# Performance work log

Hardware: AMD Instinct MI355X
Metric: run time of the kernel (lower is better)

## Reference

```python
import jax, jax.numpy as jnp
import numpy as np

N = 262144      # total atoms (ragged over batch)
B = 64          # batch_size
K = 16          # retrieved features per sample
H = 256         # h_dim
R = 512         # ret_feat_dim


def setup_inputs() -> dict:
    key = jax.random.key(0)
    k1, k2, k3, k4, k5, k6, k7 = jax.random.split(key, 7)
    h = jax.random.normal(k1, (N, H), dtype=jnp.float32)
    ret_feat = jax.random.normal(k2, (B, K, R), dtype=jnp.float32)
    batch = jnp.sort(jax.random.randint(k3, (N,), 0, B, dtype=jnp.int64))
    # nn.Linear weights: y = x @ W.T + b
    Wp = jax.random.normal(k4, (H, R), dtype=jnp.float32) / np.sqrt(R)
    bp = jax.random.normal(k5, (H,), dtype=jnp.float32) * 0.01
    Wl = jax.random.normal(k6, (H, 2 * H), dtype=jnp.float32) / np.sqrt(2 * H)
    bl = jax.random.normal(k7, (H,), dtype=jnp.float32) * 0.01
    return {"h": h, "ret_feat": ret_feat, "batch": batch,
            "Wp": Wp, "bp": bp, "Wl": Wl, "bl": bl}


def reference(h, ret_feat, batch, Wp, bp, Wl, bl):
    # ret_feat: [B, K, R] -> mean over K -> project to [B, H]
    ret = jnp.mean(ret_feat, axis=1)                    # [B, R]
    ret = ret @ Wp.T + bp                               # [B, H]
    # The torch loop gathers h[batch==i], concats the pooled feature
    # repeated per atom, applies `linear`, and scatters back. Since every
    # atom is covered exactly once, this is a per-node gather + linear:
    per_node = ret[batch]                               # [N, H] gather
    x = jnp.concatenate([h, per_node], axis=-1)         # [N, 2H]
    return x @ Wl.T + bl                                # [N, H]
```

## Files before the change

### kernel.cpp

```cpp
#include <hip/hip_runtime.h>
#include <hip/hip_bf16.h>

#define N_ATOMS 262144
#define B_SZ    64
#define H_DIM   256
#define R_DIM   512

#define TILE_ROWS 16
#define TPB       32
#define NBLOCKS   (N_ATOMS / (TILE_ROWS * TPB))
#define NBUF      4

typedef __attribute__((ext_vector_type(8))) short bf16x8;
typedef __attribute__((ext_vector_type(4))) float f32x4;

static __device__ __forceinline__ short f2bf(float f) {
  unsigned u = __builtin_bit_cast(unsigned, f);
  u = (u + 0x7FFFu + ((u >> 16) & 1u)) >> 16;
  return (short)u;
}

static __device__ __forceinline__ unsigned cvtpk(float lo, float hi) {
  unsigned r;
  asm("v_cvt_pk_bf16_f32 %0, %1, %2" : "=v"(r) : "v"(lo), "v"(hi));
  return r;
}

static __device__ __forceinline__ bf16x8 pack8(f32x4 a0, f32x4 a1) {
  unsigned u0 = cvtpk(a0[0], a0[1]);
  unsigned u1 = cvtpk(a0[2], a0[3]);
  unsigned u2 = cvtpk(a1[0], a1[1]);
  unsigned u3 = cvtpk(a1[2], a1[3]);
  bf16x8 v;
  v[0] = (short)(u0 & 0xFFFF); v[1] = (short)(u0 >> 16);
  v[2] = (short)(u1 & 0xFFFF); v[3] = (short)(u1 >> 16);
  v[4] = (short)(u2 & 0xFFFF); v[5] = (short)(u2 >> 16);
  v[6] = (short)(u3 & 0xFFFF); v[7] = (short)(u3 >> 16);
  return v;
}

static __device__ __forceinline__ void async_copy16(const float* g, short* lds) {
  __builtin_amdgcn_global_load_lds(
      (const __attribute__((address_space(1))) unsigned int*)g,
      (__attribute__((address_space(3))) unsigned int*)lds,
      16, 0, 0);
}

__global__ __launch_bounds__(1024) void prep_kernel(
    const float* __restrict__ rf, const float* __restrict__ Wp,
    const float* __restrict__ bp, const float* __restrict__ Wl,
    const float* __restrict__ bl, float* __restrict__ pooled,
    short* __restrict__ Bbf) {
  int t = threadIdx.x;
  if (blockIdx.x >= B_SZ) {
    int base = (blockIdx.x - B_SZ) * 4096 + t * 4;
#pragma unroll
    for (int q = 0; q < 4; ++q) {
      int idx  = base + q;
      int j    = idx & 7;
      int lane = (idx >> 3) & 63;
      int ks   = (idx >> 9) & 7;
      int ct   = idx >> 12;
      int o    = ct * 16 + (lane & 15);
      int k    = ks * 32 + ((lane >> 4) << 3) + j;
      Bbf[idx] = f2bf(Wl[o * (2 * H_DIM) + k]);
    }
    return;
  }

  __shared__ float meanr[R_DIM];
  __shared__ float retj[H_DIM];
  int b    = blockIdx.x;
  int lane = t & 63;
  int w    = t >> 6;

  if (t < R_DIM) {
    float s = 0.f;
    const float* p = rf + (long)b * 16 * R_DIM + t;
#pragma unroll
    for (int k = 0; k < 16; ++k) s += p[k * R_DIM];
    meanr[t] = s * (1.f / 16.f);
  }
  __syncthreads();

  {
    f32x4 m0 = *(const f32x4*)&meanr[lane * 8];
    f32x4 m1 = *(const f32x4*)&meanr[lane * 8 + 4];
#pragma unroll
    for (int jj = 0; jj < 16; ++jj) {
      int j = w * 16 + jj;
      const f32x4* wp = (const f32x4*)(Wp + (long)j * R_DIM + lane * 8);
      f32x4 w0 = wp[0], w1 = wp[1];
      float s = m0[0]*w0[0] + m0[1]*w0[1] + m0[2]*w0[2] + m0[3]*w0[3]
              + m1[0]*w1[0] + m1[1]*w1[1] + m1[2]*w1[2] + m1[3]*w1[3];
#pragma unroll
      for (int d = 1; d < 64; d <<= 1) s += __shfl_xor(s, d);
      if (lane == 0) retj[j] = s + bp[j];
    }
  }
  __syncthreads();

  {
    f32x4 r0 = *(const f32x4*)&retj[lane * 4];
#pragma unroll
    for (int oo = 0; oo < 16; ++oo) {
      int o = w * 16 + oo;
      f32x4 wv = *(const f32x4*)(Wl + (long)o * (2 * H_DIM) + H_DIM + lane * 4);
      float s = r0[0]*wv[0] + r0[1]*wv[1] + r0[2]*wv[2] + r0[3]*wv[3];
#pragma unroll
      for (int d = 1; d < 64; d <<= 1) s += __shfl_xor(s, d);
      if (lane == 0) pooled[b * H_DIM + o] = s + bl[o];
    }
  }
}

__global__ __launch_bounds__(512, 4) void gemm_kernel(
    const float* __restrict__ h, const short* __restrict__ Bbf,
    const float* __restrict__ pooled, const int* __restrict__ batch,
    float* __restrict__ out) {
  __shared__ short As[NBUF][16 * 512];
  __shared__ float pooled_lds[8 * 256];
  __shared__ short boff_lds[512];
  __shared__ short scratch[512];
  int t    = threadIdx.x;
  int lane = t & 63;
  int w    = t >> 6;
  const int arow = lane & 15;
  const int kg   = lane >> 4;

  bf16x8 bfrag0[8], bfrag1[8];
#pragma unroll
  for (int ks = 0; ks < 8; ++ks) {
    bfrag0[ks] = *(const bf16x8*)(Bbf + ((((2 * w)     * 8 + ks) * 64 + lane) << 3));
    bfrag1[ks] = *(const bf16x8*)(Bbf + ((((2 * w + 1) * 8 + ks) * 64 + lane) << 3));
  }

  long base_row = (long)blockIdx.x * (TILE_ROWS * TPB);
  int o0 = (w << 5) + (kg << 2);
  int o1 = o0 + 16;
  const long lsrc = (long)arow * H_DIM + (w << 5) + (kg << 3);

  int b_t     = batch[base_row + t];
  int b_first = batch[base_row];
  int b_last  = batch[base_row + 511];
  int span    = b_last - b_first + 1;

#pragma unroll
  for (int tl = 0; tl < 3; ++tl) {
    const float* gp = h + (base_row + (long)tl * TILE_ROWS) * H_DIM + lsrc;
    async_copy16(gp,     &As[tl][(2 * w) * 512]);
    async_copy16(gp + 4, &As[tl][(2 * w + 1) * 512]);
  }

  boff_lds[t] = (short)(b_t - b_first);
  if (span <= 8) {
    int fi = t * 4;
    if (fi < span * H_DIM)
      *(f32x4*)&pooled_lds[fi] =
          *(const f32x4*)(pooled + (long)b_first * H_DIM + fi);
  }
  asm volatile("s_waitcnt vmcnt(0) lgkmcnt(0)" ::: "memory");
  __builtin_amdgcn_s_barrier();
  __builtin_amdgcn_sched_barrier(0);

  const bool small_span = (span <= 8);

  for (int tt = 0; tt < TPB; ++tt) {
    long g0 = base_row + (long)tt * TILE_ROWS;

    {
      const float* gp;
      short *d0, *d1;
      if (tt + 3 < TPB) {
        gp = h + (g0 + 3 * TILE_ROWS) * H_DIM + lsrc;
        short* dbuf = &As[(tt + 3) & 3][0];
        d0 = dbuf + (2 * w) * 512;
        d1 = dbuf + (2 * w + 1) * 512;
      } else {
        gp = h + base_row * H_DIM + lsrc;
        d0 = scratch;
        d1 = scratch;
      }
      async_copy16(gp,     d0);
      async_copy16(gp + 4, d1);
    }
    __builtin_amdgcn_sched_barrier(0);
    asm volatile("s_waitcnt vmcnt(10)" ::: "memory");
    __builtin_amdgcn_sched_barrier(0);

    const short* ab = &As[tt & 3][0];
    f32x4 acc0 = {0.f, 0.f, 0.f, 0.f};
    f32x4 acc1 = {0.f, 0.f, 0.f, 0.f};
#pragma unroll
    for (int ks = 0; ks < 8; ++ks) {
      f32x4 v0 = *(const f32x4*)(ab + ks * 1024 + lane * 8);
      f32x4 v1 = *(const f32x4*)(ab + ks * 1024 + 512 + lane * 8);
      bf16x8 af = pack8(v0, v1);
      acc0 = __builtin_amdgcn_mfma_f32_16x16x32_bf16(bfrag0[ks], af, acc0, 0, 0, 0);
      acc1 = __builtin_amdgcn_mfma_f32_16x16x32_bf16(bfrag1[ks], af, acc1, 0, 0, 0);
    }

    int off = (int)boff_lds[tt * 16 + arow];
    f32x4 pv0, pv1;
    if (small_span) {
      pv0 = *(const f32x4*)&pooled_lds[(off << 8) + o0];
      pv1 = *(const f32x4*)&pooled_lds[(off << 8) + o1];
    } else {
      const float* pb = pooled + (long)(b_first + off) * H_DIM;
      pv0 = *(const f32x4*)(pb + o0);
      pv1 = *(const f32x4*)(pb + o1);
    }

    float* orow = out + (g0 + arow) * H_DIM;
    *(f32x4*)(orow + o0) = acc0 + pv0;
    *(f32x4*)(orow + o1) = acc1 + pv1;

    __builtin_amdgcn_s_barrier();
    __builtin_amdgcn_sched_barrier(0);
  }
}

extern "C" void kernel_launch(void* const* d_in, const int* in_sizes, int n_in,
                              void* d_out, int out_size, void* d_ws, size_t ws_size,
                              hipStream_t stream) {
  const float* h   = (const float*)d_in[0];
  const float* rf  = (const float*)d_in[1];
  const int*   bat = (const int*)d_in[2];
  const float* Wp  = (const float*)d_in[3];
  const float* bp  = (const float*)d_in[4];
  const float* Wl  = (const float*)d_in[5];
  const float* bl  = (const float*)d_in[6];
  float* out = (float*)d_out;

  float* pooled = (float*)d_ws;
  short* Bbf    = (short*)((char*)d_ws + 64 * 1024);

  prep_kernel<<<B_SZ + 16, 1024, 0, stream>>>(rf, Wp, bp, Wl, bl, pooled, Bbf);
  gemm_kernel<<<NBLOCKS, 512, 0, stream>>>(h, Bbf, pooled, bat, out);
}
```

Before: 144.8 us.

## Halve GEMM block to 4 waves, each computing four 16-column output tiles

The GEMM block shrinks from 512 to 256 threads. Each wave now holds B fragments for four 16-wide column tiles instead of two, so every converted bf16 A fragment feeds four MFMAs rather than two, and each wave loads twice as much of each h tile. The vmcnt wait moves from before the MFMA loop to after the stores, just before the barrier, so global loads can overlap more work. In exchange, register pressure rises to 128 VGPRs of B fragments, and the same LDS footprint per block means fewer resident waves per CU for hiding latency.

```diff
diff --git a/kernel.cpp b/kernel.cpp
--- a/kernel.cpp
+++ b/kernel.cpp
@@ -114,7 +114,7 @@
   }
 }
 
-__global__ __launch_bounds__(512, 4) void gemm_kernel(
+__global__ __launch_bounds__(256, 2) void gemm_kernel(
     const float* __restrict__ h, const short* __restrict__ Bbf,
     const float* __restrict__ pooled, const int* __restrict__ batch,
     float* __restrict__ out) {
@@ -128,93 +128,96 @@
   const int arow = lane & 15;
   const int kg   = lane >> 4;
 
-  bf16x8 bfrag0[8], bfrag1[8];
-#pragma unroll
-  for (int ks = 0; ks < 8; ++ks) {
-    bfrag0[ks] = *(const bf16x8*)(Bbf + ((((2 * w)     * 8 + ks) * 64 + lane) << 3));
-    bfrag1[ks] = *(const bf16x8*)(Bbf + ((((2 * w + 1) * 8 + ks) * 64 + lane) << 3));
-  }
+  bf16x8 bfrag[4][8];
+#pragma unroll
+  for (int ci = 0; ci < 4; ++ci)
+#pragma unroll
+    for (int ks = 0; ks < 8; ++ks)
+      bfrag[ci][ks] = *(const bf16x8*)(
+          Bbf + ((((4 * w + ci) * 8 + ks) * 64 + lane) << 3));
 
   long base_row = (long)blockIdx.x * (TILE_ROWS * TPB);
-  int o0 = (w << 5) + (kg << 2);
-  int o1 = o0 + 16;
-  const long lsrc = (long)arow * H_DIM + (w << 5) + (kg << 3);
+  const long lsrc = (long)arow * H_DIM + (w << 6) + (kg << 3);
 
   int b_t     = batch[base_row + t];
+  int b_t2    = batch[base_row + 256 + t];
   int b_first = batch[base_row];
-  int b_last  = batch[base_row + 511];
+  int b_last  = batch[base_row + TILE_ROWS * TPB - 1];
   int span    = b_last - b_first + 1;
-
+  boff_lds[t]       = (short)(b_t  - b_first);
+  boff_lds[t + 256] = (short)(b_t2 - b_first);
+  const bool small_span = (span <= 8);
+  if (small_span) {
+    int fi = t * 8;
+    if (fi < span * H_DIM) {
+      *(f32x4*)&pooled_lds[fi]     = *(const f32x4*)(pooled + (long)b_first * H_DIM + fi);
+      *(f32x4*)&pooled_lds[fi + 4] = *(const f32x4*)(pooled + (long)b_first * H_DIM + fi + 4);
+    }
+  }
 #pragma unroll
   for (int tl = 0; tl < 3; ++tl) {
     const float* gp = h + (base_row + (long)tl * TILE_ROWS) * H_DIM + lsrc;
-    async_copy16(gp,     &As[tl][(2 * w) * 512]);
-    async_copy16(gp + 4, &As[tl][(2 * w + 1) * 512]);
-  }
-
-  boff_lds[t] = (short)(b_t - b_first);
-  if (span <= 8) {
-    int fi = t * 4;
-    if (fi < span * H_DIM)
-      *(f32x4*)&pooled_lds[fi] =
-          *(const f32x4*)(pooled + (long)b_first * H_DIM + fi);
-  }
-  asm volatile("s_waitcnt vmcnt(0) lgkmcnt(0)" ::: "memory");
-  __builtin_amdgcn_s_barrier();
-  __builtin_amdgcn_sched_barrier(0);
-
-  const bool small_span = (span <= 8);
+    short* d = &As[tl][0];
+    async_copy16(gp,      d + (4 * w)     * 512);
+    async_copy16(gp + 4,  d + (4 * w + 1) * 512);
+    async_copy16(gp + 32, d + (4 * w + 2) * 512);
+    async_copy16(gp + 36, d + (4 * w + 3) * 512);
+  }
+  __syncthreads();
 
   for (int tt = 0; tt < TPB; ++tt) {
     long g0 = base_row + (long)tt * TILE_ROWS;
 
     {
       const float* gp;
-      short *d0, *d1;
+      short *d0, *d1, *d2, *d3;
       if (tt + 3 < TPB) {
         gp = h + (g0 + 3 * TILE_ROWS) * H_DIM + lsrc;
-        short* dbuf = &As[(tt + 3) & 3][0];
-        d0 = dbuf + (2 * w) * 512;
-        d1 = dbuf + (2 * w + 1) * 512;
+        short* d = &As[(tt + 3) & 3][0];
+        d0 = d + (4 * w)     * 512;
+        d1 = d + (4 * w + 1) * 512;
+        d2 = d + (4 * w + 2) * 512;
+        d3 = d + (4 * w + 3) * 512;
       } else {
         gp = h + base_row * H_DIM + lsrc;
-        d0 = scratch;
-        d1 = scratch;
+        d0 = d1 = d2 = d3 = scratch;
       }
-      async_copy16(gp,     d0);
-      async_copy16(gp + 4, d1);
-    }
-    __builtin_amdgcn_sched_barrier(0);
-    asm volatile("s_waitcnt vmcnt(10)" ::: "memory");
+      async_copy16(gp,      d0);
+      async_copy16(gp + 4,  d1);
+      async_copy16(gp + 32, d2);
+      async_copy16(gp + 36, d3);
+    }
     __builtin_amdgcn_sched_barrier(0);
 
     const short* ab = &As[tt & 3][0];
     f32x4 acc0 = {0.f, 0.f, 0.f, 0.f};
     f32x4 acc1 = {0.f, 0.f, 0.f, 0.f};
+    f32x4 acc2 = {0.f, 0.f, 0.f, 0.f};
+    f32x4 acc3 = {0.f, 0.f, 0.f, 0.f};
 #pragma unroll
     for (int ks = 0; ks < 8; ++ks) {
       f32x4 v0 = *(const f32x4*)(ab + ks * 1024 + lane * 8);
       f32x4 v1 = *(const f32x4*)(ab + ks * 1024 + 512 + lane * 8);
       bf16x8 af = pack8(v0, v1);
-      acc0 = __builtin_amdgcn_mfma_f32_16x16x32_bf16(bfrag0[ks], af, acc0, 0, 0, 0);
-      acc1 = __builtin_amdgcn_mfma_f32_16x16x32_bf16(bfrag1[ks], af, acc1, 0, 0, 0);
+      acc0 = __builtin_amdgcn_mfma_f32_16x16x32_bf16(bfrag[0][ks], af, acc0, 0, 0, 0);
+      acc1 = __builtin_amdgcn_mfma_f32_16x16x32_bf16(bfrag[1][ks], af, acc1, 0, 0, 0);
+      acc2 = __builtin_amdgcn_mfma_f32_16x16x32_bf16(bfrag[2][ks], af, acc2, 0, 0, 0);
+      acc3 = __builtin_amdgcn_mfma_f32_16x16x32_bf16(bfrag[3][ks], af, acc3, 0, 0, 0);
     }
 
     int off = (int)boff_lds[tt * 16 + arow];
-    f32x4 pv0, pv1;
-    if (small_span) {
-      pv0 = *(const f32x4*)&pooled_lds[(off << 8) + o0];
-      pv1 = *(const f32x4*)&pooled_lds[(off << 8) + o1];
-    } else {
-      const float* pb = pooled + (long)(b_first + off) * H_DIM;
-      pv0 = *(const f32x4*)(pb + o0);
-      pv1 = *(const f32x4*)(pb + o1);
-    }
-
+    const float* pl = small_span ? &pooled_lds[off << 8]
+                                 : pooled + (long)(b_first + off) * H_DIM;
     float* orow = out + (g0 + arow) * H_DIM;
-    *(f32x4*)(orow + o0) = acc0 + pv0;
-    *(f32x4*)(orow + o1) = acc1 + pv1;
-
+    {
+      int o = (w << 6) + (kg << 2);
+      *(f32x4*)(orow + o)      = acc0 + *(const f32x4*)(pl + o);
+      *(f32x4*)(orow + o + 16) = acc1 + *(const f32x4*)(pl + o + 16);
+      *(f32x4*)(orow + o + 32) = acc2 + *(const f32x4*)(pl + o + 32);
+      *(f32x4*)(orow + o + 48) = acc3 + *(const f32x4*)(pl + o + 48);
+    }
+
+    asm volatile("s_waitcnt vmcnt(20)" ::: "memory");
     __builtin_amdgcn_s_barrier();
     __builtin_amdgcn_sched_barrier(0);
   }
@@ -236,5 +239,5 @@
   short* Bbf    = (short*)((char*)d_ws + 64 * 1024);
 
   prep_kernel<<<B_SZ + 16, 1024, 0, stream>>>(rf, Wp, bp, Wl, bl, pooled, Bbf);
-  gemm_kernel<<<NBLOCKS, 512, 0, stream>>>(h, Bbf, pooled, bat, out);
-}
+  gemm_kernel<<<NBLOCKS, 256, 0, stream>>>(h, Bbf, pooled, bat, out);
+}
```

After: 147.4 us. Within noise of the previous version (+1.8%).
